# Optimization experiments

Hardware: AMD Instinct MI355X
Metric: run time of the kernel (lower is better)

Reference implementation:

```python
import jax, jax.numpy as jnp
import numpy as np

NUM_TAGS = 64
HIDDEN = 768
INTERMEDIATE = 3072
TAGGING_RATE = 1.0
LN_EPS = 1e-12


def layer_norm(x, g, b):
    mu = jnp.mean(x, axis=-1, keepdims=True)
    var = jnp.mean(jnp.square(x - mu), axis=-1, keepdims=True)
    return (x - mu) * jax.lax.rsqrt(var + LN_EPS) * g + b


def setup_inputs() -> dict:
    key = jax.random.key(0)
    ks = jax.random.split(key, 16)
    B, S, H, I = 8, 4096, HIDDEN, INTERMEDIATE
    s = 0.02
    return {
        "word_embedding": jax.random.normal(ks[0], (B, S, H), jnp.float32),
        "token_tags": jax.random.randint(ks[1], (B, S), 0, NUM_TAGS, jnp.int32),
        "tag_mask": jax.random.randint(ks[2], (B, S), 0, 2, jnp.int32),
        # learned params
        "tag_emb": jax.random.normal(ks[3], (NUM_TAGS, H), jnp.float32) * s,
        "Wv": jax.random.normal(ks[4], (H, H), jnp.float32) * s,   # v_proj (applied as x @ Wv)
        "bv": jnp.zeros((H,), jnp.float32),
        "Wo": jax.random.normal(ks[5], (H, H), jnp.float32) * s,   # out_proj
        "bo": jnp.zeros((H,), jnp.float32),
        "ln1_g": jnp.ones((H,), jnp.float32),
        "ln1_b": jnp.zeros((H,), jnp.float32),
        "W1": jax.random.normal(ks[6], (H, I), jnp.float32) * s,
        "b1": jnp.zeros((I,), jnp.float32),
        "W2": jax.random.normal(ks[7], (I, H), jnp.float32) * s,
        "b2": jnp.zeros((H,), jnp.float32),
        "ln2_g": jnp.ones((H,), jnp.float32),
        "ln2_b": jnp.zeros((H,), jnp.float32),
    }


def reference(word_embedding, token_tags, tag_mask, tag_emb, Wv, bv, Wo, bo,
              ln1_g, ln1_b, W1, b1, W2, b2, ln2_g, ln2_b):
    # MHA with a single key/value: softmax over one key == 1 for every head,
    # so attention_output = out_proj(v_proj(tag_embedding[tag])), independent of q.
    per_tag = (tag_emb @ Wv + bv) @ Wo + bo              # [num_tags, H]
    taged = per_tag[token_tags] * tag_mask[..., None].astype(word_embedding.dtype)  # [B,S,H]
    x = word_embedding + taged * TAGGING_RATE            # dropout is identity in eval
    x = layer_norm(x, ln1_g, ln1_b)
    ff = jax.nn.relu(x @ W1 + b1) @ W2 + b2              # feed_forward
    out = layer_norm(ff + x, ln2_g, ln2_b)
    return out
```

## Files before the change

kernel.cpp:

```cpp
#include <hip/hip_runtime.h>
#include <hip/hip_bf16.h>
#include <cstdint>
#include <cstddef>

typedef __hip_bfloat16 bf16;
typedef __attribute__((ext_vector_type(8))) short short8;
typedef __attribute__((ext_vector_type(4))) float f32x4;

__device__ __forceinline__ void gload_lds16(const void* g, void* l) {
    __builtin_amdgcn_global_load_lds((const __attribute__((address_space(1))) void*)g,
                                     (__attribute__((address_space(3))) void*)l,
                                     16, 0, 0);
}

__global__ __launch_bounds__(256)
void transpose_cvt(const float* __restrict__ in, bf16* __restrict__ out, int R, int C)
{
    __shared__ float tile[32][33];
    const int tx = threadIdx.x & 31;
    const int ty = threadIdx.x >> 5;
    const int c0 = blockIdx.x * 32;
    const int r0 = blockIdx.y * 32;
    #pragma unroll
    for (int j = 0; j < 32; j += 8)
        tile[ty + j][tx] = in[(size_t)(r0 + ty + j) * C + c0 + tx];
    __syncthreads();
    #pragma unroll
    for (int j = 0; j < 32; j += 8)
        out[(size_t)(c0 + ty + j) * R + r0 + tx] = __float2bfloat16(tile[tx][ty + j]);
}

__global__ __launch_bounds__(256)
void tag_gemm_a(const float* __restrict__ te, const float* __restrict__ Wv,
                const float* __restrict__ bv, float* __restrict__ t1)
{
    const int idx = blockIdx.x * 256 + threadIdx.x;
    const int i = idx / 768, j = idx - i * 768;
    float acc = bv[j];
    const float* a = te + (size_t)i * 768;
    for (int k = 0; k < 768; ++k)
        acc += a[k] * Wv[(size_t)k * 768 + j];
    t1[idx] = acc;
}

__global__ __launch_bounds__(256)
void tag_gemm_b(const float* __restrict__ t1, const float* __restrict__ Wo,
                const float* __restrict__ bo, float* __restrict__ ptab)
{
    const int idx = blockIdx.x * 256 + threadIdx.x;
    const int i = idx / 768, j = idx - i * 768;
    float acc = bo[j];
    const float* a = t1 + (size_t)i * 768;
    for (int k = 0; k < 768; ++k)
        acc += a[k] * Wo[(size_t)k * 768 + j];
    ptab[idx] = acc;
}

__global__ __launch_bounds__(256)
void addtag_ln(const float* __restrict__ we, const int* __restrict__ tags,
               const int* __restrict__ mask, const float* __restrict__ ptab,
               const float* __restrict__ g, const float* __restrict__ b,
               bf16* __restrict__ out)
{
    const int row = blockIdx.x;
    const int t = threadIdx.x;
    const int lane = t & 63, wid = t >> 6;
    const int tag = tags[row];
    const float msk = (float)mask[row];
    const float* wr = we + (size_t)row * 768;
    const float* pt = ptab + (size_t)tag * 768;
    float x[3];
    float s = 0.f, s2 = 0.f;
    #pragma unroll
    for (int j = 0; j < 3; ++j) {
        const int c = t + j * 256;
        const float v = wr[c] + msk * pt[c];
        x[j] = v; s += v; s2 += v * v;
    }
    #pragma unroll
    for (int o = 32; o > 0; o >>= 1) { s += __shfl_down(s, o); s2 += __shfl_down(s2, o); }
    __shared__ float ls[4], ls2[4];
    if (lane == 0) { ls[wid] = s; ls2[wid] = s2; }
    __syncthreads();
    s  = ls[0] + ls[1] + ls[2] + ls[3];
    s2 = ls2[0] + ls2[1] + ls2[2] + ls2[3];
    const float mean = s * (1.f / 768.f);
    float var = s2 * (1.f / 768.f) - mean * mean;
    var = var < 0.f ? 0.f : var;
    const float inv = 1.f / sqrtf(var + 1e-12f);
    bf16* orow = out + (size_t)row * 768;
    #pragma unroll
    for (int j = 0; j < 3; ++j) {
        const int c = t + j * 256;
        orow[c] = __float2bfloat16((x[j] - mean) * inv * g[c] + b[c]);
    }
}

__global__ __launch_bounds__(256)
void ln_inplace(float* __restrict__ y, const float* __restrict__ g, const float* __restrict__ b)
{
    const int row = blockIdx.x;
    const int t = threadIdx.x;
    const int lane = t & 63, wid = t >> 6;
    float* yr = y + (size_t)row * 768;
    float x[3];
    float s = 0.f, s2 = 0.f;
    #pragma unroll
    for (int j = 0; j < 3; ++j) {
        const int c = t + j * 256;
        const float v = yr[c];
        x[j] = v; s += v; s2 += v * v;
    }
    #pragma unroll
    for (int o = 32; o > 0; o >>= 1) { s += __shfl_down(s, o); s2 += __shfl_down(s2, o); }
    __shared__ float ls[4], ls2[4];
    if (lane == 0) { ls[wid] = s; ls2[wid] = s2; }
    __syncthreads();
    s  = ls[0] + ls[1] + ls[2] + ls[3];
    s2 = ls2[0] + ls2[1] + ls2[2] + ls2[3];
    const float mean = s * (1.f / 768.f);
    float var = s2 * (1.f / 768.f) - mean * mean;
    var = var < 0.f ? 0.f : var;
    const float inv = 1.f / sqrtf(var + 1e-12f);
    #pragma unroll
    for (int j = 0; j < 3; ++j) {
        const int c = t + j * 256;
        yr[c] = (x[j] - mean) * inv * g[c] + b[c];
    }
}

template<int EPI, typename OutT>
__global__ __launch_bounds__(256)
void gemm128(const bf16* __restrict__ A, const bf16* __restrict__ Bt,
             const float* __restrict__ bias, const bf16* __restrict__ resid,
             OutT* __restrict__ C, int N, int K)
{
    __shared__ bf16 As[128 * 64];
    __shared__ bf16 Bs[128 * 64];
    const int t = threadIdx.x;
    const int lane = t & 63;
    const int wid  = t >> 6;
    const int quad = lane >> 4;
    const int lr   = lane & 15;
    const int rowBase = blockIdx.y * 128;
    const int colBase = blockIdx.x * 128;
    const int wm = (wid >> 1) * 64;
    const int wn = (wid & 1) * 64;

    f32x4 acc[4][4] = {};

    const char* Ab = (const char*)(A + (size_t)rowBase * K);
    const char* Bb = (const char*)(Bt + (size_t)colBase * K);
    const int strideBytes = K * 2;
    char* AsB = (char*)As;
    char* BsB = (char*)Bs;

    int srow[4], soff[4];
    #pragma unroll
    for (int p = 0; p < 4; ++p) {
        const int i = t + p * 256;
        srow[p] = i >> 3;
        soff[p] = ((i & 7) ^ (srow[p] & 7)) * 16;
    }

    for (int kt = 0; kt < K; kt += 64) {
        const int kb = kt * 2;
        #pragma unroll
        for (int p = 0; p < 4; ++p) {
            const int i = t + p * 256;
            gload_lds16(Ab + (size_t)srow[p] * strideBytes + kb + soff[p], AsB + i * 16);
            gload_lds16(Bb + (size_t)srow[p] * strideBytes + kb + soff[p], BsB + i * 16);
        }
        __syncthreads();
        #pragma unroll
        for (int j = 0; j < 2; ++j) {
            const int cch = j * 4 + quad;
            short8 af[4], bfr[4];
            #pragma unroll
            for (int mi = 0; mi < 4; ++mi) {
                const int R = wm + mi * 16 + lr;
                af[mi] = *(const short8*)(AsB + R * 128 + ((cch ^ (R & 7)) * 16));
            }
            #pragma unroll
            for (int ni = 0; ni < 4; ++ni) {
                const int R = wn + ni * 16 + lr;
                bfr[ni] = *(const short8*)(BsB + R * 128 + ((cch ^ (R & 7)) * 16));
            }
            #pragma unroll
            for (int mi = 0; mi < 4; ++mi) {
                #pragma unroll
                for (int ni = 0; ni < 4; ++ni)
                    acc[mi][ni] = __builtin_amdgcn_mfma_f32_16x16x32_bf16(
                        af[mi], bfr[ni], acc[mi][ni], 0, 0, 0);
            }
        }
        __syncthreads();
    }

    #pragma unroll
    for (int ni = 0; ni < 4; ++ni) {
        const int gc = colBase + wn + ni * 16 + lr;
        const float bvv = bias[gc];
        #pragma unroll
        for (int mi = 0; mi < 4; ++mi) {
            const int gr0 = rowBase + wm + mi * 16 + quad * 4;
            #pragma unroll
            for (int r = 0; r < 4; ++r) {
                const size_t off = (size_t)(gr0 + r) * N + gc;
                float v = acc[mi][ni][r] + bvv;
                if (EPI == 0) {
                    v = v > 0.f ? v : 0.f;
                    C[off] = (OutT)__float2bfloat16(v);
                } else {
                    v += (float)resid[off];
                    C[off] = (OutT)v;
                }
            }
        }
    }
}

extern "C" void kernel_launch(void* const* d_in, const int* in_sizes, int n_in,
                              void* d_out, int out_size, void* d_ws, size_t ws_size,
                              hipStream_t stream)
{
    const float* we      = (const float*)d_in[0];
    const int*   tags    = (const int*)d_in[1];
    const int*   mask    = (const int*)d_in[2];
    const float* tag_emb = (const float*)d_in[3];
    const float* Wv      = (const float*)d_in[4];
    const float* bv      = (const float*)d_in[5];
    const float* Wo      = (const float*)d_in[6];
    const float* bo      = (const float*)d_in[7];
    const float* ln1g    = (const float*)d_in[8];
    const float* ln1b    = (const float*)d_in[9];
    const float* W1      = (const float*)d_in[10];
    const float* b1      = (const float*)d_in[11];
    const float* W2      = (const float*)d_in[12];
    const float* b2      = (const float*)d_in[13];
    const float* ln2g    = (const float*)d_in[14];
    const float* ln2b    = (const float*)d_in[15];
    float* out = (float*)d_out;

    const int M = 8 * 4096;
    char* ws = (char*)d_ws;
    const size_t oT1   = 0;
    const size_t oPtab = 196608;
    const size_t oW1t  = 393216;
    const size_t oW2t  = 5111808;
    const size_t oXn   = 9830400;
    const size_t oHh   = 60162048;
    const size_t hhFull = (size_t)M * 3072 * 2;

    const int nchunk = (ws_size >= oHh + hhFull) ? 1 : 2;
    const int MC = M / nchunk;

    float* t1   = (float*)(ws + oT1);
    float* ptab = (float*)(ws + oPtab);
    bf16*  W1t  = (bf16*)(ws + oW1t);
    bf16*  W2t  = (bf16*)(ws + oW2t);
    bf16*  xn   = (bf16*)(ws + oXn);
    bf16*  hh   = (bf16*)(ws + oHh);

    transpose_cvt<<<dim3(3072 / 32, 768 / 32), 256, 0, stream>>>(W1, W1t, 768, 3072);
    transpose_cvt<<<dim3(768 / 32, 3072 / 32), 256, 0, stream>>>(W2, W2t, 3072, 768);

    tag_gemm_a<<<192, 256, 0, stream>>>(tag_emb, Wv, bv, t1);
    tag_gemm_b<<<192, 256, 0, stream>>>(t1, Wo, bo, ptab);

    addtag_ln<<<M, 256, 0, stream>>>(we, tags, mask, ptab, ln1g, ln1b, xn);

    for (int c = 0; c < nchunk; ++c) {
        const bf16* xnC = xn + (size_t)c * MC * 768;
        gemm128<0, bf16><<<dim3(3072 / 128, MC / 128), 256, 0, stream>>>(
            xnC, W1t, b1, nullptr, hh, 3072, 768);
        gemm128<1, float><<<dim3(768 / 128, MC / 128), 256, 0, stream>>>(
            hh, W2t, b2, xnC, out + (size_t)c * MC * 768, 768, 3072);
    }

    ln_inplace<<<M, 256, 0, stream>>>(out, ln2g, ln2b);
}
```

Baseline: 821.0 us.

## Load GEMM A-fragments directly to registers, swizzle block order, fuse tag GEMMs

The GEMM kernel stops staging A tiles in LDS. Each wave now loads its A fragments straight from global memory into registers, while B still goes through LDS. Block IDs are remapped into a grouped order to improve L2 reuse, and launch bounds ask for 3 blocks per CU. The two tag-table GEMV kernels are fused into one 64-block kernel that keeps the intermediate row in shared memory. Direct global A loads lose coalescing and reuse across waves, and the tag kernel now runs with far fewer blocks.

```diff
diff --git a/kernel.cpp b/kernel.cpp
--- a/kernel.cpp
+++ b/kernel.cpp
@@ -31,29 +31,31 @@
 }
 
 __global__ __launch_bounds__(256)
-void tag_gemm_a(const float* __restrict__ te, const float* __restrict__ Wv,
-                const float* __restrict__ bv, float* __restrict__ t1)
-{
-    const int idx = blockIdx.x * 256 + threadIdx.x;
-    const int i = idx / 768, j = idx - i * 768;
-    float acc = bv[j];
-    const float* a = te + (size_t)i * 768;
-    for (int k = 0; k < 768; ++k)
-        acc += a[k] * Wv[(size_t)k * 768 + j];
-    t1[idx] = acc;
-}
-
-__global__ __launch_bounds__(256)
-void tag_gemm_b(const float* __restrict__ t1, const float* __restrict__ Wo,
-                const float* __restrict__ bo, float* __restrict__ ptab)
-{
-    const int idx = blockIdx.x * 256 + threadIdx.x;
-    const int i = idx / 768, j = idx - i * 768;
-    float acc = bo[j];
-    const float* a = t1 + (size_t)i * 768;
-    for (int k = 0; k < 768; ++k)
-        acc += a[k] * Wo[(size_t)k * 768 + j];
-    ptab[idx] = acc;
+void tag_table(const float* __restrict__ te, const float* __restrict__ Wv,
+               const float* __restrict__ bv, const float* __restrict__ Wo,
+               const float* __restrict__ bo, float* __restrict__ ptab)
+{
+    __shared__ float t1s[768];
+    const int i = blockIdx.x;
+    const int t = threadIdx.x;
+    const float* ter = te + (size_t)i * 768;
+    #pragma unroll
+    for (int jj = 0; jj < 3; ++jj) {
+        const int j = t + jj * 256;
+        float acc = bv[j];
+        for (int k = 0; k < 768; ++k)
+            acc += ter[k] * Wv[(size_t)k * 768 + j];
+        t1s[j] = acc;
+    }
+    __syncthreads();
+    #pragma unroll
+    for (int jj = 0; jj < 3; ++jj) {
+        const int j = t + jj * 256;
+        float acc = bo[j];
+        for (int k = 0; k < 768; ++k)
+            acc += t1s[k] * Wo[(size_t)k * 768 + j];
+        ptab[(size_t)i * 768 + j] = acc;
+    }
 }
 
 __global__ __launch_bounds__(256)
@@ -130,30 +132,37 @@
 }
 
 template<int EPI, typename OutT>
-__global__ __launch_bounds__(256)
+__global__ __launch_bounds__(256, 3)
 void gemm128(const bf16* __restrict__ A, const bf16* __restrict__ Bt,
              const float* __restrict__ bias, const bf16* __restrict__ resid,
              OutT* __restrict__ C, int N, int K)
 {
-    __shared__ bf16 As[128 * 64];
     __shared__ bf16 Bs[128 * 64];
     const int t = threadIdx.x;
     const int lane = t & 63;
     const int wid  = t >> 6;
     const int quad = lane >> 4;
     const int lr   = lane & 15;
-    const int rowBase = blockIdx.y * 128;
-    const int colBase = blockIdx.x * 128;
+
+    const int gx = gridDim.x;
+    const int bid = blockIdx.y * gx + blockIdx.x;
+    const int slot = bid >> 3;
+    const int rl = slot / gx;
+    const int colB = slot - rl * gx;
+    const int rowB = (bid & 7) * (gridDim.y >> 3) + rl;
+    const int rowBase = rowB * 128;
+    const int colBase = colB * 128;
+
     const int wm = (wid >> 1) * 64;
     const int wn = (wid & 1) * 64;
 
     f32x4 acc[4][4] = {};
 
+    const int strideBytes = K * 2;
     const char* Ab = (const char*)(A + (size_t)rowBase * K);
     const char* Bb = (const char*)(Bt + (size_t)colBase * K);
-    const int strideBytes = K * 2;
-    char* AsB = (char*)As;
     char* BsB = (char*)Bs;
+    const char* aPtr = Ab + (size_t)(wm + lr) * strideBytes + quad * 16;
 
     int srow[4], soff[4];
     #pragma unroll
@@ -168,19 +177,19 @@
         #pragma unroll
         for (int p = 0; p < 4; ++p) {
             const int i = t + p * 256;
-            gload_lds16(Ab + (size_t)srow[p] * strideBytes + kb + soff[p], AsB + i * 16);
             gload_lds16(Bb + (size_t)srow[p] * strideBytes + kb + soff[p], BsB + i * 16);
         }
+        short8 af[4][2];
+        #pragma unroll
+        for (int mi = 0; mi < 4; ++mi)
+            #pragma unroll
+            for (int jj = 0; jj < 2; ++jj)
+                af[mi][jj] = *(const short8*)(aPtr + (size_t)mi * 16 * strideBytes + kb + jj * 64);
         __syncthreads();
         #pragma unroll
-        for (int j = 0; j < 2; ++j) {
-            const int cch = j * 4 + quad;
-            short8 af[4], bfr[4];
-            #pragma unroll
-            for (int mi = 0; mi < 4; ++mi) {
-                const int R = wm + mi * 16 + lr;
-                af[mi] = *(const short8*)(AsB + R * 128 + ((cch ^ (R & 7)) * 16));
-            }
+        for (int jj = 0; jj < 2; ++jj) {
+            const int cch = jj * 4 + quad;
+            short8 bfr[4];
             #pragma unroll
             for (int ni = 0; ni < 4; ++ni) {
                 const int R = wn + ni * 16 + lr;
@@ -191,7 +200,7 @@
                 #pragma unroll
                 for (int ni = 0; ni < 4; ++ni)
                     acc[mi][ni] = __builtin_amdgcn_mfma_f32_16x16x32_bf16(
-                        af[mi], bfr[ni], acc[mi][ni], 0, 0, 0);
+                        af[mi][jj], bfr[ni], acc[mi][ni], 0, 0, 0);
             }
         }
         __syncthreads();
@@ -244,18 +253,16 @@
 
     const int M = 8 * 4096;
     char* ws = (char*)d_ws;
-    const size_t oT1   = 0;
-    const size_t oPtab = 196608;
-    const size_t oW1t  = 393216;
-    const size_t oW2t  = 5111808;
-    const size_t oXn   = 9830400;
-    const size_t oHh   = 60162048;
+    const size_t oPtab = 0;
+    const size_t oW1t  = 196608;
+    const size_t oW2t  = 4915200;
+    const size_t oXn   = 9633792;
+    const size_t oHh   = 59965440;
     const size_t hhFull = (size_t)M * 3072 * 2;
 
     const int nchunk = (ws_size >= oHh + hhFull) ? 1 : 2;
     const int MC = M / nchunk;
 
-    float* t1   = (float*)(ws + oT1);
     float* ptab = (float*)(ws + oPtab);
     bf16*  W1t  = (bf16*)(ws + oW1t);
     bf16*  W2t  = (bf16*)(ws + oW2t);
@@ -265,8 +272,7 @@
     transpose_cvt<<<dim3(3072 / 32, 768 / 32), 256, 0, stream>>>(W1, W1t, 768, 3072);
     transpose_cvt<<<dim3(768 / 32, 3072 / 32), 256, 0, stream>>>(W2, W2t, 3072, 768);
 
-    tag_gemm_a<<<192, 256, 0, stream>>>(tag_emb, Wv, bv, t1);
-    tag_gemm_b<<<192, 256, 0, stream>>>(t1, Wo, bo, ptab);
+    tag_table<<<64, 256, 0, stream>>>(tag_emb, Wv, bv, Wo, bo, ptab);
 
     addtag_ln<<<M, 256, 0, stream>>>(we, tags, mask, ptab, ln1g, ln1b, xn);
 
```

Result: slower. 1.184 ms (+44.2%).
